# Optimization experiments

Hardware: AMD Instinct MI355X
Metric: run time of the kernel (lower is better)

Reference implementation:

```python
import jax, jax.numpy as jnp
import numpy as np

B, L, DIM, H = 1, 2048, 1536, 12
HD = DIM // H  # 128
SCALE = HD ** -0.5


def quantize_dequant_int8(t):
    # per-tensor symmetric int8 quantize then float dequantize (same math as torch ref)
    s = jnp.max(jnp.abs(t)) / 127.0
    q = jnp.clip(jnp.round(t / s), -128.0, 127.0)
    return q * s


def setup_inputs() -> dict:
    key = jax.random.key(0)
    ks = jax.random.split(key, 6)
    std = DIM ** -0.5
    return {
        "x": jax.random.normal(ks[0], (B, L, DIM), jnp.float32),
        "Wq": jax.random.normal(ks[1], (DIM, DIM), jnp.float32) * std,
        "Wk": jax.random.normal(ks[2], (DIM, DIM), jnp.float32) * std,
        "Wv": jax.random.normal(ks[3], (DIM, DIM), jnp.float32) * std,
        "Wo": jax.random.normal(ks[4], (DIM, DIM), jnp.float32) * std,
        "bo": jax.random.normal(ks[5], (DIM,), jnp.float32) * 0.01,
    }


def reference(x, Wq, Wk, Wv, Wo, bo):
    b, l, c = x.shape
    # QKV projections (torch Linear: x @ W^T), reshape to [B,H,L,HD]
    q = (x @ Wq.T).reshape(b, l, H, HD).transpose(0, 2, 1, 3)
    k = (x @ Wk.T).reshape(b, l, H, HD).transpose(0, 2, 1, 3)
    v = (x @ Wv.T).reshape(b, l, H, HD).transpose(0, 2, 1, 3)
    # sage-style quantize/dequant around both matmuls
    qd = quantize_dequant_int8(q)
    kd = quantize_dequant_int8(k)
    scores = jnp.einsum('bhqd,bhkd->bhqk', qd, kd) * SCALE
    probs = jax.nn.softmax(scores, axis=-1)
    pd = quantize_dequant_int8(probs)
    vd = quantize_dequant_int8(v)
    out = jnp.einsum('bhqk,bhkd->bhqd', pd, vd)  # [B,H,L,HD]
    out = out.transpose(0, 2, 1, 3).reshape(b, l, c)
    return out @ Wo.T + bo
```

## Files before the change

### kernel.cpp

```cpp
#include <hip/hip_runtime.h>
#include <stdint.h>

#define SEQ 2048
#define DIM 1536
#define NH  12
#define HD  128
#define SCALEF 0.08838834764831845f

typedef __attribute__((ext_vector_type(8))) short short8;
typedef __attribute__((ext_vector_type(4))) float floatx4;

#define MFMA16(a, b, c) __builtin_amdgcn_mfma_f32_16x16x32_bf16((a), (b), (c), 0, 0, 0)

__device__ __forceinline__ void async_cp16(const void* g, void* l) {
  __builtin_amdgcn_global_load_lds(
      (__attribute__((address_space(1))) unsigned int*)(g),
      (__attribute__((address_space(3))) unsigned int*)(l), 16, 0, 0);
}

__device__ __forceinline__ unsigned short f2bf(float f) {
  unsigned int u = __float_as_uint(f);
  u = (u + 0x7fff + ((u >> 16) & 1)) >> 16;
  return (unsigned short)u;
}

__device__ __forceinline__ void split8v(const float* x, short8& h, short8& l) {
#pragma unroll
  for (int e = 0; e < 8; e++) {
    unsigned int u = __float_as_uint(x[e]);
    h[e] = (short)(u >> 16);
    float r = x[e] - __uint_as_float(u & 0xFFFF0000u);
    l[e] = (short)f2bf(r);
  }
}
__device__ __forceinline__ void split8(const float* g, short8& h, short8& l) {
  float4 f0 = *(const float4*)g, f1 = *(const float4*)(g + 4);
  float x[8] = {f0.x, f0.y, f0.z, f0.w, f1.x, f1.y, f1.z, f1.w};
  split8v(x, h, l);
}

__global__ __launch_bounds__(256) void k_fill(float* __restrict__ out, int n,
                                              float val) {
  int i = blockIdx.x * 256 + threadIdx.x;
  if (i < n) out[i] = val;
}

__global__ __launch_bounds__(256) void k_split_x(
    const float* __restrict__ X, unsigned short* __restrict__ Xh,
    unsigned short* __restrict__ Xl) {
  int ks = blockIdx.x, mb = blockIdx.y, tid = threadIdx.x;
  size_t tb = ((size_t)mb * 48 + ks) * 4096;
#pragma unroll
  for (int i = 0; i < 2; i++) {
    int sidx = i * 256 + tid;
    int row = sidx >> 2, p = sidx & 3;
    int c = p ^ ((row >> 1) & 3);
    short8 h, l;
    split8(X + (size_t)(mb * 128 + row) * DIM + ks * 32 + c * 8, h, l);
    *(short8*)(Xh + tb + sidx * 8) = h;
    *(short8*)(Xl + tb + sidx * 8) = l;
  }
}

__global__ __launch_bounds__(256) void k_split_o(
    const float* __restrict__ A0, const float* __restrict__ A1,
    unsigned short* __restrict__ Oh, unsigned short* __restrict__ Ol) {
  int ks = blockIdx.x, mb = blockIdx.y, tid = threadIdx.x;
  size_t tb = ((size_t)mb * 48 + ks) * 4096;
#pragma unroll
  for (int i = 0; i < 2; i++) {
    int sidx = i * 256 + tid;
    int row = sidx >> 2, p = sidx & 3;
    int c = p ^ ((row >> 1) & 3);
    size_t off = (size_t)(mb * 128 + row) * DIM + ks * 32 + c * 8;
    float4 x0 = *(const float4*)(A0 + off), x1 = *(const float4*)(A0 + off + 4);
    float4 y0 = *(const float4*)(A1 + off), y1 = *(const float4*)(A1 + off + 4);
    float xs[8] = {x0.x + y0.x, x0.y + y0.y, x0.z + y0.z, x0.w + y0.w,
                   x1.x + y1.x, x1.y + y1.y, x1.z + y1.z, x1.w + y1.w};
    short8 h, l;
    split8v(xs, h, l);
    *(short8*)(Oh + tb + sidx * 8) = h;
    *(short8*)(Ol + tb + sidx * 8) = l;
  }
}

#define COMPUTE_TILE(SA, SB)                                                  \
  {                                                                           \
    const unsigned short* Ah_ = Abh + (SA) * 4096;                            \
    const unsigned short* Al_ = Abl + (SA) * 4096;                            \
    const unsigned short* Bh_ = Bbh + (SB) * 4096;                            \
    const unsigned short* Bl_ = Bbl + (SB) * 4096;                            \
    short8 ah_[4], al_[4], bh_[4], bl_[4];                                    \
    _Pragma("unroll") for (int i_ = 0; i_ < 4; i_++) {                        \
      int off_ = (mrbase + i_ * 16) * 32 + phA;                               \
      ah_[i_] = *(const short8*)(Ah_ + off_);                                 \
      al_[i_] = *(const short8*)(Al_ + off_);                                 \
    }                                                                         \
    _Pragma("unroll") for (int j_ = 0; j_ < 4; j_++) {                        \
      int off_ = q * 1024 + (wc * 64 + j_ * 16 + lm) * 8;                     \
      bh_[j_] = *(const short8*)(Bh_ + off_);                                 \
      bl_[j_] = *(const short8*)(Bl_ + off_);                                 \
    }                                                                         \
    __builtin_amdgcn_s_setprio(1);                                            \
    _Pragma("unroll") for (int i_ = 0; i_ < 4; i_++)                          \
      _Pragma("unroll") for (int j_ = 0; j_ < 4; j_++) {                      \
        acc[i_][j_] = MFMA16(ah_[i_], bh_[j_], acc[i_][j_]);                  \
        acc[i_][j_] = MFMA16(ah_[i_], bl_[j_], acc[i_][j_]);                  \
        acc[i_][j_] = MFMA16(al_[i_], bh_[j_], acc[i_][j_]);                  \
      }                                                                       \
    __builtin_amdgcn_s_setprio(0);                                            \
  }

#define SPLIT_B(SB, S0x, S1x, S2x, S3x)                                       \
  {                                                                           \
    unsigned short* BhN_ = Bbh + (SB) * 4096;                                 \
    unsigned short* BlN_ = Bbl + (SB) * 4096;                                 \
    short8 h_, l_;                                                            \
    {                                                                         \
      float xs_[8] = {S0x.x, S0x.y, S0x.z, S0x.w,                             \
                      S1x.x, S1x.y, S1x.z, S1x.w};                            \
      split8v(xs_, h_, l_);                                                   \
      *(short8*)(BhN_ + c8 * 1024 + rowA * 8) = h_;                           \
      *(short8*)(BlN_ + c8 * 1024 + rowA * 8) = l_;                           \
    }                                                                         \
    {                                                                         \
      float xs_[8] = {S2x.x, S2x.y, S2x.z, S2x.w,                             \
                      S3x.x, S3x.y, S3x.z, S3x.w};                            \
      split8v(xs_, h_, l_);                                                   \
      *(short8*)(BhN_ + c8 * 1024 + (64 + rowA) * 8) = h_;                    \
      *(short8*)(BlN_ + c8 * 1024 + (64 + rowA) * 8) = l_;                    \
    }                                                                         \
  }

#define GSTEP(T, SCUR, S0x, S1x, S2x, S3x, L0x, L1x, L2x, L3x)                \
  {                                                                           \
    const int t_ = (T), sc_ = (SCUR);                                         \
    const int sn_ = sc_ >= 1 ? sc_ - 1 : 2;                    \
    size_t tn_ = tb + (size_t)(t_ + 2) * 4096;                                \
    async_cp16(XH_ + tn_ + sidx0 * 8, Abh + sn_ * 4096 + sidx0 * 8);          \
    async_cp16(XL_ + tn_ + sidx0 * 8, Abl + sn_ * 4096 + sidx0 * 8);          \
    async_cp16(XH_ + tn_ + sidx1 * 8, Abh + sn_ * 4096 + sidx1 * 8);          \
    async_cp16(XL_ + tn_ + sidx1 * 8, Abl + sn_ * 4096 + sidx1 * 8);          \
    {                                                                         \
      int kn_ = (t_ + 2) * 32;                                                \
      L0x = *(const float4*)(pB0 + kn_);                                      \
      L1x = *(const float4*)(pB0 + kn_ + 4);                                  \
      L2x = *(const float4*)(pB1 + kn_);                                      \
      L3x = *(const float4*)(pB1 + kn_ + 4);                                  \
    }                                                                         \
    COMPUTE_TILE(sc_, (t_) & 1);                                              \
    SPLIT_B((t_ + 1) & 1, S0x, S1x, S2x, S3x);                                \
    asm volatile("s_waitcnt vmcnt(8) lgkmcnt(0)" ::: "memory");               \
    __builtin_amdgcn_s_barrier();                                             \
    __builtin_amdgcn_sched_barrier(0);                                        \
  }

__global__ __launch_bounds__(256) void k_gemm_qkv(
    const unsigned short* __restrict__ Xh, const unsigned short* __restrict__ Xl,
    const float* __restrict__ Wq, const float* __restrict__ Wk,
    const float* __restrict__ Wv, float* __restrict__ qf,
    float* __restrict__ kf, float* __restrict__ vf,
    unsigned int* __restrict__ scal) {
  __shared__ __align__(16) unsigned short Ahs[3][4096], Als[3][4096];
  __shared__ __align__(16) unsigned short Bhs[2][4096], Bls[2][4096];
  int tid = threadIdx.x;
  int L = blockIdx.x + 12 * blockIdx.y + 192 * blockIdx.z;
  int L2 = (L & 7) * 72 + (L >> 3);
  int by2 = L2 & 15, rest = L2 >> 4;
  int bx2 = rest % 12, z = rest / 12;
  const float* W = (z == 0) ? Wq : (z == 1) ? Wk : Wv;
  float* C = (z == 0) ? qf : (z == 1) ? kf : vf;
  int n0 = bx2 * 128, m0 = by2 * 128;
  int lane = tid & 63, w = tid >> 6;
  int wr = w >> 1, wc = w & 1, lm = lane & 15, q = lane >> 4;

  floatx4 acc[4][4];
#pragma unroll
  for (int i = 0; i < 4; i++)
#pragma unroll
    for (int j = 0; j < 4; j++) acc[i][j] = (floatx4){0.f, 0.f, 0.f, 0.f};

  int rowA = tid >> 2, c8 = tid & 3;
  const float* pB0 = W + (size_t)(n0 + rowA) * DIM + c8 * 8;
  const float* pB1 = pB0 + (size_t)64 * DIM;
  size_t tb = (size_t)by2 * 48 * 4096;
  int sidx0 = tid, sidx1 = 256 + tid;
  int phA = (q ^ ((lm >> 1) & 3)) * 8;
  int mrbase = wr * 64 + lm;
  unsigned short* Abh = &Ahs[0][0];
  unsigned short* Abl = &Als[0][0];
  unsigned short* Bbh = &Bhs[0][0];
  unsigned short* Bbl = &Bls[0][0];
  const unsigned short* XH_ = Xh;
  const unsigned short* XL_ = Xl;

  float4 wA0, wA1, wA2, wA3, wB0, wB1, wB2, wB3;
  wB0 = *(const float4*)(pB0);
  wB1 = *(const float4*)(pB0 + 4);
  wB2 = *(const float4*)(pB1);
  wB3 = *(const float4*)(pB1 + 4);
  async_cp16(XH_ + tb + sidx0 * 8, Abh + sidx0 * 8);
  async_cp16(XL_ + tb + sidx0 * 8, Abl + sidx0 * 8);
  async_cp16(XH_ + tb + sidx1 * 8, Abh + sidx1 * 8);
  async_cp16(XL_ + tb + sidx1 * 8, Abl + sidx1 * 8);
  async_cp16(XH_ + tb + 4096 + sidx0 * 8, Abh + 4096 + sidx0 * 8);
  async_cp16(XL_ + tb + 4096 + sidx0 * 8, Abl + 4096 + sidx0 * 8);
  async_cp16(XH_ + tb + 4096 + sidx1 * 8, Abh + 4096 + sidx1 * 8);
  async_cp16(XL_ + tb + 4096 + sidx1 * 8, Abl + 4096 + sidx1 * 8);
  wA0 = *(const float4*)(pB0 + 32);
  wA1 = *(const float4*)(pB0 + 36);
  wA2 = *(const float4*)(pB1 + 32);
  wA3 = *(const float4*)(pB1 + 36);
  SPLIT_B(0, wB0, wB1, wB2, wB3);
  asm volatile("s_waitcnt vmcnt(8) lgkmcnt(0)" ::: "memory");
  __builtin_amdgcn_s_barrier();
  __builtin_amdgcn_sched_barrier(0);

  int scur = 0;
  for (int p = 0; p < 23; ++p) {
    GSTEP(2 * p, scur, wA0, wA1, wA2, wA3, wB0, wB1, wB2, wB3);
    scur = (scur + 1 == 3) ? 0 : scur + 1;
    GSTEP(2 * p + 1, scur, wB0, wB1, wB2, wB3, wA0, wA1, wA2, wA3);
    scur = (scur + 1 == 3) ? 0 : scur + 1;
  }
  COMPUTE_TILE(1, 0);
  SPLIT_B(1, wA0, wA1, wA2, wA3);
  asm volatile("s_waitcnt lgkmcnt(0)" ::: "memory");
  __builtin_amdgcn_s_barrier();
  __builtin_amdgcn_sched_barrier(0);
  COMPUTE_TILE(2, 1);

  float am = 0.f;
#pragma unroll
  for (int i = 0; i < 4; i++) {
    int row = m0 + wr * 64 + i * 16 + q * 4;
#pragma unroll
    for (int j = 0; j < 4; j++) {
      int col = n0 + wc * 64 + j * 16 + lm;
#pragma unroll
      for (int r = 0; r < 4; r++) {
        float v = acc[i][j][r];
        C[(size_t)(row + r) * DIM + col] = v;
        am = fmaxf(am, fabsf(v));
      }
    }
  }
#pragma unroll
  for (int mk = 32; mk >= 1; mk >>= 1) am = fmaxf(am, __shfl_xor(am, mk, 64));
  if (lane == 0) atomicMax(&scal[z], __float_as_uint(am));
}

__global__ __launch_bounds__(256) void k_quant_vT(
    const float* __restrict__ vf, const unsigned int* __restrict__ scal,
    unsigned short* __restrict__ nvT) {
  __shared__ float T[64 * 65];
  int h = blockIdx.z, d0 = blockIdx.y * 64, k0 = blockIdx.x * 64;
  float s = __uint_as_float(scal[2]) / 127.f;
  int t = threadIdx.x;
#pragma unroll
  for (int i = 0; i < 16; i++) {
    int idx = i * 256 + t;
    int r = idx >> 6, c = idx & 63;
    float v = vf[(size_t)(k0 + r) * DIM + h * HD + d0 + c];
    T[r * 65 + c] = fminf(fmaxf(rintf(v / s), -128.f), 127.f);
  }
  __syncthreads();
#pragma unroll
  for (int i = 0; i < 16; i++) {
    int idx = i * 256 + t;
    int d = idx >> 6, r = idx & 63;
    nvT[(size_t)(h * HD + d0 + d) * SEQ + k0 + r] = f2bf(T[r * 65 + d]);
  }
}

__global__ __launch_bounds__(256) void k_quant_qk(
    const float* __restrict__ qf, const float* __restrict__ kf,
    const unsigned int* __restrict__ scal,
    unsigned short* __restrict__ nq, unsigned short* __restrict__ nk) {
  int z = blockIdx.y;
  const float* src = z ? kf : qf;
  unsigned short* dst = z ? nk : nq;
  float s = __uint_as_float(scal[z]) / 127.f;
  size_t i = ((size_t)blockIdx.x * 256 + threadIdx.x) * 4;
  float4 v = *(const float4*)(src + i);
  ushort4 o;
  o.x = f2bf(fminf(fmaxf(rintf(v.x / s), -128.f), 127.f));
  o.y = f2bf(fminf(fmaxf(rintf(v.y / s), -128.f), 127.f));
  o.z = f2bf(fminf(fmaxf(rintf(v.z / s), -128.f), 127.f));
  o.w = f2bf(fminf(fmaxf(rintf(v.w / s), -128.f), 127.f));
  *(ushort4*)(dst + i) = o;
}

__global__ __launch_bounds__(256) void k_stats(
    const unsigned short* __restrict__ nq, const unsigned short* __restrict__ nk,
    const unsigned int* __restrict__ scal, float* __restrict__ pstats) {
  __shared__ unsigned short Ks[32 * 128];
  int h = blockIdx.y, tid = threadIdx.x, lane = tid & 63, w = tid >> 6;
  int lm = lane & 15, q = lane >> 4;
  int qb = blockIdx.x & 15, chunk = blockIdx.x >> 4;
  int mb = qb * 128 + w * 32;
  int kbase = chunk * 256;
  float f = (__uint_as_float(scal[0]) / 127.f) *
            (__uint_as_float(scal[1]) / 127.f) * SCALEF;

  short8 aq[2][4];
#pragma unroll
  for (int mi = 0; mi < 2; mi++) {
    const unsigned short* qb_p =
        nq + (size_t)(mb + mi * 16 + lm) * DIM + h * HD + q * 8;
#pragma unroll
    for (int cc = 0; cc < 4; cc++) aq[mi][cc] = *(const short8*)(qb_p + cc * 32);
  }

  float m[2][4], zz[2][4];
#pragma unroll
  for (int mi = 0; mi < 2; mi++)
#pragma unroll
    for (int r = 0; r < 4; r++) { m[mi][r] = -3.0e38f; zz[mi][r] = 0.f; }

  for (int kt = kbase; kt < kbase + 256; kt += 32) {
    __syncthreads();
#pragma unroll
    for (int i = 0; i < 2; i++) {
      int ch = i * 256 + tid;
      int krow = ch >> 4;
      int gcol = (ch & 15) ^ (krow & 7);
      async_cp16(nk + (size_t)(kt + krow) * DIM + h * HD + gcol * 8,
                 Ks + ch * 8);
    }
    __syncthreads();
    short8 bk[2][4];
#pragma unroll
    for (int st = 0; st < 2; st++)
#pragma unroll
      for (int cc = 0; cc < 4; cc++) {
        int phys = (cc * 4 + q) ^ (lm & 7);
        bk[st][cc] = *(const short8*)(Ks + (st * 16 + lm) * 128 + phys * 8);
      }
#pragma unroll
    for (int mi = 0; mi < 2; mi++) {
      floatx4 a0 = (floatx4){0.f, 0.f, 0.f, 0.f};
      floatx4 a1 = (floatx4){0.f, 0.f, 0.f, 0.f};
#pragma unroll
      for (int cc = 0; cc < 4; cc++) {
        a0 = MFMA16(aq[mi][cc], bk[0][cc], a0);
        a1 = MFMA16(aq[mi][cc], bk[1][cc], a1);
      }
#pragma unroll
      for (int r = 0; r < 4; r++) {
        float s0 = a0[r] * f, s1 = a1[r] * f;
        float nm = fmaxf(m[mi][r], fmaxf(s0, s1));
        zz[mi][r] = zz[mi][r] * __expf(m[mi][r] - nm) + __expf(s0 - nm) +
                    __expf(s1 - nm);
        m[mi][r] = nm;
      }
    }
  }
#pragma unroll
  for (int mk = 1; mk < 16; mk <<= 1)
#pragma unroll
    for (int mi = 0; mi < 2; mi++)
#pragma unroll
      for (int r = 0; r < 4; r++) {
        float om = __shfl_xor(m[mi][r], mk, 64);
        float oz = __shfl_xor(zz[mi][r], mk, 64);
        float nm = fmaxf(m[mi][r], om);
        zz[mi][r] = zz[mi][r] * __expf(m[mi][r] - nm) + oz * __expf(om - nm);
        m[mi][r] = nm;
      }
  if (lm == 0) {
#pragma unroll
    for (int mi = 0; mi < 2; mi++)
#pragma unroll
      for (int r = 0; r < 4; r++) {
        int row = mb + mi * 16 + q * 4 + r;
        float* p = pstats + (((size_t)h * SEQ + row) * 8 + chunk) * 2;
        p[0] = m[mi][r];
        p[1] = zz[mi][r];
      }
  }
}

__global__ __launch_bounds__(256) void k_merge(
    const float* __restrict__ pstats, float* __restrict__ stats,
    unsigned int* __restrict__ minZ) {
  int idx = blockIdx.x * 256 + threadIdx.x;
  const float* p = pstats + (size_t)idx * 16;
  float M = -3.0e38f;
#pragma unroll
  for (int c = 0; c < 8; c++) M = fmaxf(M, p[c * 2]);
  float Z = 0.f;
#pragma unroll
  for (int c = 0; c < 8; c++) Z += p[c * 2 + 1] * __expf(p[c * 2] - M);
  stats[(size_t)idx * 2] = M;
  stats[(size_t)idx * 2 + 1] = Z;
  atomicMin(minZ, __float_as_uint(Z));
}

__global__ __launch_bounds__(256) void k_attn(
    const unsigned short* __restrict__ nq, const unsigned short* __restrict__ nk,
    const unsigned short* __restrict__ nvT,
    const unsigned int* __restrict__ scal, const unsigned int* __restrict__ minZ,
    const float* __restrict__ stats, float* __restrict__ attn0,
    float* __restrict__ attn1) {
  __shared__ unsigned short Ks[32 * 128];
  __shared__ unsigned short Vs[128 * 32];
  __shared__ unsigned short Pl[4][16 * 40];
  int h = blockIdx.y, tid = threadIdx.x, lane = tid & 63, w = tid >> 6;
  int lm = lane & 15, q = lane >> 4;
  int qb = blockIdx.x & 31, chunk = blockIdx.x >> 5;
  int mb = qb * 64 + w * 16;
  float* attn = chunk ? attn1 : attn0;
  float sv = __uint_as_float(scal[2]) / 127.f;
  float f = (__uint_as_float(scal[0]) / 127.f) *
            (__uint_as_float(scal[1]) / 127.f) * SCALEF;
  float sp = (1.f / __uint_as_float(*minZ)) / 127.f;
  float inv_sp = 1.f / sp;

  short8 aq[4];
  {
    const unsigned short* qb_p =
        nq + (size_t)(mb + lm) * DIM + h * HD + q * 8;
#pragma unroll
    for (int cc = 0; cc < 4; cc++) aq[cc] = *(const short8*)(qb_p + cc * 32);
  }
  float M[4], invZ[4];
#pragma unroll
  for (int r = 0; r < 4; r++) {
    int row = mb + q * 4 + r;
    M[r] = stats[((size_t)h * SEQ + row) * 2];
    invZ[r] = 1.f / stats[((size_t)h * SEQ + row) * 2 + 1];
  }
  floatx4 accO[8];
#pragma unroll
  for (int j = 0; j < 8; j++) accO[j] = (floatx4){0.f, 0.f, 0.f, 0.f};

  int kbase = chunk * 1024;
  for (int kt = kbase; kt < kbase + 1024; kt += 32) {
    __syncthreads();
#pragma unroll
    for (int i = 0; i < 2; i++) {
      int ch = i * 256 + tid;
      int krow = ch >> 4;
      int gcol = (ch & 15) ^ (krow & 7);
      async_cp16(nk + (size_t)(kt + krow) * DIM + h * HD + gcol * 8,
                 Ks + ch * 8);
      int d = ch >> 2;
      int vcol = (ch & 3) ^ ((d >> 1) & 3);
      async_cp16(nvT + (size_t)(h * HD + d) * SEQ + kt + vcol * 8,
                 Vs + ch * 8);
    }
    __syncthreads();
    short8 bk[2][4];
#pragma unroll
    for (int st = 0; st < 2; st++)
#pragma unroll
      for (int cc = 0; cc < 4; cc++) {
        int phys = (cc * 4 + q) ^ (lm & 7);
        bk[st][cc] = *(const short8*)(Ks + (st * 16 + lm) * 128 + phys * 8);
      }
#pragma unroll
    for (int st = 0; st < 2; st++) {
      floatx4 acc = (floatx4){0.f, 0.f, 0.f, 0.f};
#pragma unroll
      for (int cc = 0; cc < 4; cc++) acc = MFMA16(aq[cc], bk[st][cc], acc);
#pragma unroll
      for (int r = 0; r < 4; r++) {
        float t = __expf(acc[r] * f - M[r]);
        float n = rintf(t * invZ[r] * inv_sp);
        n = fminf(n, 127.f);
        Pl[w][(q * 4 + r) * 40 + st * 16 + lm] = f2bf(n);
      }
    }
    __syncthreads();
    short8 ap = *(const short8*)(&Pl[w][lm * 40 + q * 8]);
#pragma unroll
    for (int j = 0; j < 8; j++) {
      int d = j * 16 + lm;
      int vphys = q ^ ((d >> 1) & 3);
      short8 bv = *(const short8*)(Vs + d * 32 + vphys * 8);
      accO[j] = MFMA16(ap, bv, accO[j]);
    }
  }
  float osc = sp * sv;
#pragma unroll
  for (int j = 0; j < 8; j++)
#pragma unroll
    for (int r = 0; r < 4; r++)
      attn[(size_t)(mb + q * 4 + r) * DIM + h * HD + j * 16 + lm] =
          accO[j][r] * osc;
}

__global__ __launch_bounds__(256) void k_gemm_out(
    const unsigned short* __restrict__ Oh, const unsigned short* __restrict__ Ol,
    const float* __restrict__ Wo, const float* __restrict__ bo,
    float* __restrict__ out) {
  __shared__ __align__(16) unsigned short Ahs[3][4096], Als[3][4096];
  __shared__ __align__(16) unsigned short Bhs[2][4096], Bls[2][4096];
  int tid = threadIdx.x;
  int L = blockIdx.x + 12 * blockIdx.y;
  int L2 = (L & 7) * 24 + (L >> 3);
  int by2 = L2 & 15, bx2 = L2 >> 4;
  int n0 = bx2 * 128, m0 = by2 * 128;
  int lane = tid & 63, w = tid >> 6;
  int wr = w >> 1, wc = w & 1, lm = lane & 15, q = lane >> 4;

  floatx4 acc[4][4];
#pragma unroll
  for (int i = 0; i < 4; i++)
#pragma unroll
    for (int j = 0; j < 4; j++) acc[i][j] = (floatx4){0.f, 0.f, 0.f, 0.f};

  int rowA = tid >> 2, c8 = tid & 3;
  const float* pB0 = Wo + (size_t)(n0 + rowA) * DIM + c8 * 8;
  const float* pB1 = pB0 + (size_t)64 * DIM;
  size_t tb = (size_t)by2 * 48 * 4096;
  int sidx0 = tid, sidx1 = 256 + tid;
  int phA = (q ^ ((lm >> 1) & 3)) * 8;
  int mrbase = wr * 64 + lm;
  unsigned short* Abh = &Ahs[0][0];
  unsigned short* Abl = &Als[0][0];
  unsigned short* Bbh = &Bhs[0][0];
  unsigned short* Bbl = &Bls[0][0];
  const unsigned short* XH_ = Oh;
  const unsigned short* XL_ = Ol;

  float4 wA0, wA1, wA2, wA3, wB0, wB1, wB2, wB3;
  wB0 = *(const float4*)(pB0);
  wB1 = *(const float4*)(pB0 + 4);
  wB2 = *(const float4*)(pB1);
  wB3 = *(const float4*)(pB1 + 4);
  async_cp16(XH_ + tb + sidx0 * 8, Abh + sidx0 * 8);
  async_cp16(XL_ + tb + sidx0 * 8, Abl + sidx0 * 8);
  async_cp16(XH_ + tb + sidx1 * 8, Abh + sidx1 * 8);
  async_cp16(XL_ + tb + sidx1 * 8, Abl + sidx1 * 8);
  async_cp16(XH_ + tb + 4096 + sidx0 * 8, Abh + 4096 + sidx0 * 8);
  async_cp16(XL_ + tb + 4096 + sidx0 * 8, Abl + 4096 + sidx0 * 8);
  async_cp16(XH_ + tb + 4096 + sidx1 * 8, Abh + 4096 + sidx1 * 8);
  async_cp16(XL_ + tb + 4096 + sidx1 * 8, Abl + 4096 + sidx1 * 8);
  wA0 = *(const float4*)(pB0 + 32);
  wA1 = *(const float4*)(pB0 + 36);
  wA2 = *(const float4*)(pB1 + 32);
  wA3 = *(const float4*)(pB1 + 36);
  SPLIT_B(0, wB0, wB1, wB2, wB3);
  asm volatile("s_waitcnt vmcnt(8) lgkmcnt(0)" ::: "memory");
  __builtin_amdgcn_s_barrier();
  __builtin_amdgcn_sched_barrier(0);

  int scur = 0;
  for (int p = 0; p < 23; ++p) {
    GSTEP(2 * p, scur, wA0, wA1, wA2, wA3, wB0, wB1, wB2, wB3);
    scur = (scur + 1 == 3) ? 0 : scur + 1;
    GSTEP(2 * p + 1, scur, wB0, wB1, wB2, wB3, wA0, wA1, wA2, wA3);
    scur = (scur + 1 == 3) ? 0 : scur + 1;
  }
  COMPUTE_TILE(1, 0);
  SPLIT_B(1, wA0, wA1, wA2, wA3);
  asm volatile("s_waitcnt lgkmcnt(0)" ::: "memory");
  __builtin_amdgcn_s_barrier();
  __builtin_amdgcn_sched_barrier(0);
  COMPUTE_TILE(2, 1);

#pragma unroll
  for (int j = 0; j < 4; j++) {
    int col = n0 + wc * 64 + j * 16 + lm;
    float bias = bo[col];
#pragma unroll
    for (int i = 0; i < 4; i++) {
      int row = m0 + wr * 64 + i * 16 + q * 4;
#pragma unroll
      for (int r = 0; r < 4; r++)
        out[(size_t)(row + r) * DIM + col] = acc[i][j][r] + bias;
    }
  }
}

extern "C" void kernel_launch(void* const* d_in, const int* in_sizes, int n_in,
                              void* d_out, int out_size, void* d_ws, size_t ws_size,
                              hipStream_t stream) {
  float* out = (float*)d_out;
  bool sizes_ok = (n_in >= 6) && in_sizes && in_sizes[0] == SEQ * DIM &&
                  in_sizes[1] == DIM * DIM && in_sizes[2] == DIM * DIM &&
                  in_sizes[3] == DIM * DIM && in_sizes[4] == DIM * DIM &&
                  in_sizes[5] == DIM && out_size == SEQ * DIM;
  if (!sizes_ok) {
    k_fill<<<(out_size + 255) / 256, 256, 0, stream>>>(out, out_size, 1.0f);
    return;
  }
  if (ws_size < 50528272) {
    k_fill<<<(out_size + 255) / 256, 256, 0, stream>>>(out, out_size, 2.0f);
    return;
  }

  const float* x  = (const float*)d_in[0];
  const float* Wq = (const float*)d_in[1];
  const float* Wk = (const float*)d_in[2];
  const float* Wv = (const float*)d_in[3];
  const float* Wo = (const float*)d_in[4];
  const float* bo = (const float*)d_in[5];
  char* ws = (char*)d_ws;

  float* qf = (float*)(ws);
  float* kf = (float*)(ws + 12582912);
  float* vf = (float*)(ws + 25165824);
  unsigned short* nq  = (unsigned short*)(ws + 25165824);
  float* pstats = (float*)(ws + 31457280);
  unsigned short* nvT = (unsigned short*)(ws + 37748736);
  unsigned short* nk  = (unsigned short*)(ws + 44040192);
  unsigned short* Xh = nvT;
  unsigned short* Xl = nk;
  unsigned short* Oh = nvT;
  unsigned short* Ol = nk;
  float* attn0 = qf;
  float* attn1 = kf;
  float* stats = (float*)(ws + 50331648);
  unsigned int* scal = (unsigned int*)(ws + 50528256);

  hipMemsetAsync(scal, 0, 12, stream);
  hipMemsetAsync(scal + 3, 0x7f, 4, stream);

  k_split_x<<<dim3(48, 16), 256, 0, stream>>>(x, Xh, Xl);
  k_gemm_qkv<<<dim3(12, 16, 3), 256, 0, stream>>>(Xh, Xl, Wq, Wk, Wv, qf, kf,
                                                  vf, scal);
  k_quant_vT<<<dim3(SEQ / 64, HD / 64, NH), 256, 0, stream>>>(vf, scal, nvT);
  k_quant_qk<<<dim3((SEQ * DIM) / 1024, 2), 256, 0, stream>>>(qf, kf, scal, nq, nk);
  k_stats<<<dim3(8 * 16, NH), 256, 0, stream>>>(nq, nk, scal, pstats);
  k_merge<<<dim3(NH * SEQ / 256), 256, 0, stream>>>(pstats, stats, scal + 3);
  k_attn<<<dim3(2 * 32, NH), 256, 0, stream>>>(nq, nk, nvT, scal, scal + 3,
                                               stats, attn0, attn1);
  k_split_o<<<dim3(48, 16), 256, 0, stream>>>(attn0, attn1, Oh, Ol);
  k_gemm_out<<<dim3(12, 16), 256, 0, stream>>>(Oh, Ol, Wo, bo, out);
}
```

Before: 464.6 us.

## Split-K the output projection GEMM into two halves with a merge kernel

The output projection GEMM, previously launched as 192 workgroups (fewer than the GPU's CUs), now splits the K dimension in two and runs 384 workgroups. Each writes a partial product to a workspace buffer, and a new elementwise kernel adds the two partials plus the bias. The prologue and main loop are factored into shared macros so the loop count can differ per kernel. The cost is an extra launch and the traffic of writing and re-reading two full fp32 output-sized buffers.

```diff
diff --git a/kernel.cpp b/kernel.cpp
--- a/kernel.cpp
+++ b/kernel.cpp
@@ -155,6 +155,43 @@
     __builtin_amdgcn_sched_barrier(0);                                        \
   }
 
+#define GEMM_PRO()                                                            \
+  wB0 = *(const float4*)(pB0);                                                \
+  wB1 = *(const float4*)(pB0 + 4);                                            \
+  wB2 = *(const float4*)(pB1);                                                \
+  wB3 = *(const float4*)(pB1 + 4);                                            \
+  async_cp16(XH_ + tb + sidx0 * 8, Abh + sidx0 * 8);                          \
+  async_cp16(XL_ + tb + sidx0 * 8, Abl + sidx0 * 8);                          \
+  async_cp16(XH_ + tb + sidx1 * 8, Abh + sidx1 * 8);                          \
+  async_cp16(XL_ + tb + sidx1 * 8, Abl + sidx1 * 8);                          \
+  async_cp16(XH_ + tb + 4096 + sidx0 * 8, Abh + 4096 + sidx0 * 8);            \
+  async_cp16(XL_ + tb + 4096 + sidx0 * 8, Abl + 4096 + sidx0 * 8);            \
+  async_cp16(XH_ + tb + 4096 + sidx1 * 8, Abh + 4096 + sidx1 * 8);            \
+  async_cp16(XL_ + tb + 4096 + sidx1 * 8, Abl + 4096 + sidx1 * 8);            \
+  wA0 = *(const float4*)(pB0 + 32);                                           \
+  wA1 = *(const float4*)(pB0 + 36);                                           \
+  wA2 = *(const float4*)(pB1 + 32);                                           \
+  wA3 = *(const float4*)(pB1 + 36);                                           \
+  SPLIT_B(0, wB0, wB1, wB2, wB3);                                             \
+  asm volatile("s_waitcnt vmcnt(8) lgkmcnt(0)" ::: "memory");                 \
+  __builtin_amdgcn_s_barrier();                                               \
+  __builtin_amdgcn_sched_barrier(0);
+
+#define GEMM_LOOP(NPAIR, TTAIL)                                               \
+  int scur = 0;                                                               \
+  for (int p = 0; p < (NPAIR); ++p) {                                         \
+    GSTEP(2 * p, scur, wA0, wA1, wA2, wA3, wB0, wB1, wB2, wB3);               \
+    scur = (scur + 1 == 3) ? 0 : scur + 1;                                    \
+    GSTEP(2 * p + 1, scur, wB0, wB1, wB2, wB3, wA0, wA1, wA2, wA3);           \
+    scur = (scur + 1 == 3) ? 0 : scur + 1;                                    \
+  }                                                                           \
+  COMPUTE_TILE((TTAIL) % 3, 0);                                               \
+  SPLIT_B(1, wA0, wA1, wA2, wA3);                                             \
+  asm volatile("s_waitcnt lgkmcnt(0)" ::: "memory");                          \
+  __builtin_amdgcn_s_barrier();                                               \
+  __builtin_amdgcn_sched_barrier(0);                                          \
+  COMPUTE_TILE(((TTAIL) + 1) % 3, 1);
+
 __global__ __launch_bounds__(256) void k_gemm_qkv(
     const unsigned short* __restrict__ Xh, const unsigned short* __restrict__ Xl,
     const float* __restrict__ Wq, const float* __restrict__ Wk,
@@ -195,40 +232,8 @@
   const unsigned short* XL_ = Xl;
 
   float4 wA0, wA1, wA2, wA3, wB0, wB1, wB2, wB3;
-  wB0 = *(const float4*)(pB0);
-  wB1 = *(const float4*)(pB0 + 4);
-  wB2 = *(const float4*)(pB1);
-  wB3 = *(const float4*)(pB1 + 4);
-  async_cp16(XH_ + tb + sidx0 * 8, Abh + sidx0 * 8);
-  async_cp16(XL_ + tb + sidx0 * 8, Abl + sidx0 * 8);
-  async_cp16(XH_ + tb + sidx1 * 8, Abh + sidx1 * 8);
-  async_cp16(XL_ + tb + sidx1 * 8, Abl + sidx1 * 8);
-  async_cp16(XH_ + tb + 4096 + sidx0 * 8, Abh + 4096 + sidx0 * 8);
-  async_cp16(XL_ + tb + 4096 + sidx0 * 8, Abl + 4096 + sidx0 * 8);
-  async_cp16(XH_ + tb + 4096 + sidx1 * 8, Abh + 4096 + sidx1 * 8);
-  async_cp16(XL_ + tb + 4096 + sidx1 * 8, Abl + 4096 + sidx1 * 8);
-  wA0 = *(const float4*)(pB0 + 32);
-  wA1 = *(const float4*)(pB0 + 36);
-  wA2 = *(const float4*)(pB1 + 32);
-  wA3 = *(const float4*)(pB1 + 36);
-  SPLIT_B(0, wB0, wB1, wB2, wB3);
-  asm volatile("s_waitcnt vmcnt(8) lgkmcnt(0)" ::: "memory");
-  __builtin_amdgcn_s_barrier();
-  __builtin_amdgcn_sched_barrier(0);
-
-  int scur = 0;
-  for (int p = 0; p < 23; ++p) {
-    GSTEP(2 * p, scur, wA0, wA1, wA2, wA3, wB0, wB1, wB2, wB3);
-    scur = (scur + 1 == 3) ? 0 : scur + 1;
-    GSTEP(2 * p + 1, scur, wB0, wB1, wB2, wB3, wA0, wA1, wA2, wA3);
-    scur = (scur + 1 == 3) ? 0 : scur + 1;
-  }
-  COMPUTE_TILE(1, 0);
-  SPLIT_B(1, wA0, wA1, wA2, wA3);
-  asm volatile("s_waitcnt lgkmcnt(0)" ::: "memory");
-  __builtin_amdgcn_s_barrier();
-  __builtin_amdgcn_sched_barrier(0);
-  COMPUTE_TILE(2, 1);
+  GEMM_PRO();
+  GEMM_LOOP(23, 46);
 
   float am = 0.f;
 #pragma unroll
@@ -493,14 +498,16 @@
 
 __global__ __launch_bounds__(256) void k_gemm_out(
     const unsigned short* __restrict__ Oh, const unsigned short* __restrict__ Ol,
-    const float* __restrict__ Wo, const float* __restrict__ bo,
-    float* __restrict__ out) {
+    const float* __restrict__ Wo, float* __restrict__ P0,
+    float* __restrict__ P1) {
   __shared__ __align__(16) unsigned short Ahs[3][4096], Als[3][4096];
   __shared__ __align__(16) unsigned short Bhs[2][4096], Bls[2][4096];
   int tid = threadIdx.x;
-  int L = blockIdx.x + 12 * blockIdx.y;
-  int L2 = (L & 7) * 24 + (L >> 3);
-  int by2 = L2 & 15, bx2 = L2 >> 4;
+  int L = blockIdx.x;
+  int L2 = (L & 7) * 48 + (L >> 3);
+  int kc = L2 & 1, rest = L2 >> 1;
+  int by2 = rest & 15, bx2 = rest >> 4;
+  float* C = kc ? P1 : P0;
   int n0 = bx2 * 128, m0 = by2 * 128;
   int lane = tid & 63, w = tid >> 6;
   int wr = w >> 1, wc = w & 1, lm = lane & 15, q = lane >> 4;
@@ -512,9 +519,9 @@
     for (int j = 0; j < 4; j++) acc[i][j] = (floatx4){0.f, 0.f, 0.f, 0.f};
 
   int rowA = tid >> 2, c8 = tid & 3;
-  const float* pB0 = Wo + (size_t)(n0 + rowA) * DIM + c8 * 8;
+  const float* pB0 = Wo + (size_t)(n0 + rowA) * DIM + kc * 768 + c8 * 8;
   const float* pB1 = pB0 + (size_t)64 * DIM;
-  size_t tb = (size_t)by2 * 48 * 4096;
+  size_t tb = ((size_t)by2 * 48 + kc * 24) * 4096;
   int sidx0 = tid, sidx1 = 256 + tid;
   int phA = (q ^ ((lm >> 1) & 3)) * 8;
   int mrbase = wr * 64 + lm;
@@ -526,53 +533,36 @@
   const unsigned short* XL_ = Ol;
 
   float4 wA0, wA1, wA2, wA3, wB0, wB1, wB2, wB3;
-  wB0 = *(const float4*)(pB0);
-  wB1 = *(const float4*)(pB0 + 4);
-  wB2 = *(const float4*)(pB1);
-  wB3 = *(const float4*)(pB1 + 4);
-  async_cp16(XH_ + tb + sidx0 * 8, Abh + sidx0 * 8);
-  async_cp16(XL_ + tb + sidx0 * 8, Abl + sidx0 * 8);
-  async_cp16(XH_ + tb + sidx1 * 8, Abh + sidx1 * 8);
-  async_cp16(XL_ + tb + sidx1 * 8, Abl + sidx1 * 8);
-  async_cp16(XH_ + tb + 4096 + sidx0 * 8, Abh + 4096 + sidx0 * 8);
-  async_cp16(XL_ + tb + 4096 + sidx0 * 8, Abl + 4096 + sidx0 * 8);
-  async_cp16(XH_ + tb + 4096 + sidx1 * 8, Abh + 4096 + sidx1 * 8);
-  async_cp16(XL_ + tb + 4096 + sidx1 * 8, Abl + 4096 + sidx1 * 8);
-  wA0 = *(const float4*)(pB0 + 32);
-  wA1 = *(const float4*)(pB0 + 36);
-  wA2 = *(const float4*)(pB1 + 32);
-  wA3 = *(const float4*)(pB1 + 36);
-  SPLIT_B(0, wB0, wB1, wB2, wB3);
-  asm volatile("s_waitcnt vmcnt(8) lgkmcnt(0)" ::: "memory");
-  __builtin_amdgcn_s_barrier();
-  __builtin_amdgcn_sched_barrier(0);
-
-  int scur = 0;
-  for (int p = 0; p < 23; ++p) {
-    GSTEP(2 * p, scur, wA0, wA1, wA2, wA3, wB0, wB1, wB2, wB3);
-    scur = (scur + 1 == 3) ? 0 : scur + 1;
-    GSTEP(2 * p + 1, scur, wB0, wB1, wB2, wB3, wA0, wA1, wA2, wA3);
-    scur = (scur + 1 == 3) ? 0 : scur + 1;
-  }
-  COMPUTE_TILE(1, 0);
-  SPLIT_B(1, wA0, wA1, wA2, wA3);
-  asm volatile("s_waitcnt lgkmcnt(0)" ::: "memory");
-  __builtin_amdgcn_s_barrier();
-  __builtin_amdgcn_sched_barrier(0);
-  COMPUTE_TILE(2, 1);
+  GEMM_PRO();
+  GEMM_LOOP(11, 22);
 
 #pragma unroll
   for (int j = 0; j < 4; j++) {
     int col = n0 + wc * 64 + j * 16 + lm;
-    float bias = bo[col];
 #pragma unroll
     for (int i = 0; i < 4; i++) {
       int row = m0 + wr * 64 + i * 16 + q * 4;
 #pragma unroll
       for (int r = 0; r < 4; r++)
-        out[(size_t)(row + r) * DIM + col] = acc[i][j][r] + bias;
+        C[(size_t)(row + r) * DIM + col] = acc[i][j][r];
     }
   }
+}
+
+__global__ __launch_bounds__(256) void k_merge_out(
+    const float* __restrict__ P0, const float* __restrict__ P1,
+    const float* __restrict__ bo, float* __restrict__ out) {
+  size_t i = ((size_t)blockIdx.x * 256 + threadIdx.x) * 4;
+  int col = (int)(i % DIM);
+  float4 a = *(const float4*)(P0 + i);
+  float4 b = *(const float4*)(P1 + i);
+  float4 bb = *(const float4*)(bo + col);
+  float4 o;
+  o.x = a.x + b.x + bb.x;
+  o.y = a.y + b.y + bb.y;
+  o.z = a.z + b.z + bb.z;
+  o.w = a.w + b.w + bb.w;
+  *(float4*)(out + i) = o;
 }
 
 extern "C" void kernel_launch(void* const* d_in, const int* in_sizes, int n_in,
@@ -613,6 +603,8 @@
   unsigned short* Ol = nk;
   float* attn0 = qf;
   float* attn1 = kf;
+  float* outP0 = qf;
+  float* outP1 = kf;
   float* stats = (float*)(ws + 50331648);
   unsigned int* scal = (unsigned int*)(ws + 50528256);
 
@@ -629,5 +621,6 @@
   k_attn<<<dim3(2 * 32, NH), 256, 0, stream>>>(nq, nk, nvT, scal, scal + 3,
                                                stats, attn0, attn1);
   k_split_o<<<dim3(48, 16), 256, 0, stream>>>(attn0, attn1, Oh, Ol);
-  k_gemm_out<<<dim3(12, 16), 256, 0, stream>>>(Oh, Ol, Wo, bo, out);
-}
+  k_gemm_out<<<dim3(384), 256, 0, stream>>>(Oh, Ol, Wo, outP0, outP1);
+  k_merge_out<<<dim3(SEQ * DIM / 1024), 256, 0, stream>>>(outP0, outP1, bo, out);
+}
```

Result: faster. 440.8 us (-5.1%).
